# Performance work log

Measured on AMD Instinct MI355X. Metric: run time of the kernel, lower is better.

The kernel has to match this reference:

```python
import jax, jax.numpy as jnp
import numpy as np
import math

N_HEAD = 16

def _rope_tables(seq, dh, dtype):
    inv_freq = 1.0 / (10000.0 ** (jnp.arange(0, dh, 2, dtype=jnp.float32) / dh))
    angle = jnp.arange(seq, dtype=jnp.float32)[:, None] * inv_freq[None, :]  # [S, dh/2]
    sin = jnp.repeat(jnp.sin(angle), 2, axis=-1).astype(dtype)  # [S, dh]
    cos = jnp.repeat(jnp.cos(angle), 2, axis=-1).astype(dtype)
    return sin, cos

def _rotate_half(x):
    x_even = x[..., ::2]
    x_odd = x[..., 1::2]
    return jnp.stack([-x_odd, x_even], axis=-1).reshape(x.shape)

def _apply_rope(x, sin, cos):
    # x: [B, H, S, dh]; sin/cos: [S, dh]
    return x * cos[None, None] + _rotate_half(x) * sin[None, None]

def setup_inputs() -> dict:
    key = jax.random.key(0)
    ks = jax.random.split(key, 9)
    B, S, D = 2, 2048, 2048
    scale = 1.0 / math.sqrt(D)
    x = jax.random.normal(ks[0], (B, S, D), dtype=jnp.float32)
    wq = jax.random.normal(ks[1], (D, D), dtype=jnp.float32) * scale
    wk = jax.random.normal(ks[2], (D, D), dtype=jnp.float32) * scale
    wv = jax.random.normal(ks[3], (D, D), dtype=jnp.float32) * scale
    wo = jax.random.normal(ks[4], (D, D), dtype=jnp.float32) * scale
    bq = jnp.zeros((D,), jnp.float32)
    bk = jnp.zeros((D,), jnp.float32)
    bv = jnp.zeros((D,), jnp.float32)
    bo = jnp.zeros((D,), jnp.float32)
    # causal mask: True = masked (strict upper triangle)
    mask = jnp.triu(jnp.ones((S, S), dtype=bool), k=1)[None, None]  # [1,1,S,S]
    return {"x": x, "wq": wq, "bq": bq, "wk": wk, "bk": bk, "wv": wv, "bv": bv,
            "wo": wo, "bo": bo, "mask": mask}

def reference(x, wq, bq, wk, bk, wv, bv, wo, bo, mask):
    B, S, D = x.shape
    H = N_HEAD
    dh = D // H
    # projections (torch Linear: x @ W.T + b)
    q = (x @ wq.T + bq).reshape(B, S, H, dh).transpose(0, 2, 1, 3)  # [B,H,S,dh]
    k = (x @ wk.T + bk).reshape(B, S, H, dh).transpose(0, 2, 1, 3)
    v = (x @ wv.T + bv).reshape(B, S, H, dh).transpose(0, 2, 1, 3)
    sin, cos = _rope_tables(S, dh, x.dtype)
    q = _apply_rope(q, sin, cos)
    k = _apply_rope(k, sin, cos)
    scores = jnp.einsum('bhqd,bhkd->bhqk', q, k) / math.sqrt(dh)
    scores = jnp.where(mask, -jnp.inf, scores)
    attn = jax.nn.softmax(scores, axis=-1)
    attn = jnp.nan_to_num(attn, nan=0.0)
    out = jnp.einsum('bhqk,bhkd->bhqd', attn, v)  # [B,H,S,dh]
    out = out.transpose(0, 2, 1, 3).reshape(B, S, D)
    return out @ wo.T + bo
```

## Files before the change

kernel.cpp:

```cpp
#include <hip/hip_runtime.h>
#include <math.h>


typedef _Float16 half8 __attribute__((ext_vector_type(8)));
typedef _Float16 half4v __attribute__((ext_vector_type(4)));
typedef float f32x4 __attribute__((ext_vector_type(4)));

__device__ __forceinline__ void gl_lds16(const void* g, void* l) {
  __builtin_amdgcn_global_load_lds(
      (const __attribute__((address_space(1))) unsigned int*)g,
      (__attribute__((address_space(3))) unsigned int*)l, 16, 0, 0);
}

__global__ void cast_f32_f16(const float* __restrict__ src, _Float16* __restrict__ dst, int n4) {
  int i = blockIdx.x * blockDim.x + threadIdx.x;
  if (i >= n4) return;
  float4 v = reinterpret_cast<const float4*>(src)[i];
  half4v o;
  o[0] = (_Float16)v.x; o[1] = (_Float16)v.y; o[2] = (_Float16)v.z; o[3] = (_Float16)v.w;
  reinterpret_cast<half4v*>(dst)[i] = o;
}

__global__ void cast_w(const float* __restrict__ w0, const float* __restrict__ w1,
                       const float* __restrict__ w2, const float* __restrict__ w3,
                       _Float16* __restrict__ wdst) {
  const float* s = blockIdx.y == 0 ? w0 : blockIdx.y == 1 ? w1 : blockIdx.y == 2 ? w2 : w3;
  int i = blockIdx.x * blockDim.x + threadIdx.x;
  float4 v = reinterpret_cast<const float4*>(s)[i];
  half4v o;
  o[0] = (_Float16)v.x; o[1] = (_Float16)v.y; o[2] = (_Float16)v.z; o[3] = (_Float16)v.w;
  reinterpret_cast<half4v*>(wdst)[(size_t)blockIdx.y * 1048576 + i] = o;
}

template <bool OUT_F32>
__global__ __launch_bounds__(256, 2) void gemm_bt_big(
    const _Float16* __restrict__ A,
    const _Float16* __restrict__ B,
    const float* __restrict__ b0, const float* __restrict__ b1,
    const float* __restrict__ b2,
    void* __restrict__ Cout,
    int M, int N, int K) {
  __shared__ _Float16 As[2][4096];
  __shared__ _Float16 Bs[2][8192];
  const int bm = blockIdx.y * 128, bn = blockIdx.x * 256;
  const int tid = threadIdx.x;
  const int wave = tid >> 6, lane = tid & 63;
  const int quad = lane >> 4, l16 = lane & 15;
  const int ih = wave >> 1, jh = wave & 1;

  const _Float16* gsrc[6];
  int lofs[6];
#pragma unroll
  for (int p = 0; p < 6; ++p) {
    if (p < 2) {
      int c = p * 256 + tid;
      int cl16 = c & 15, cqd = (c >> 4) & 3, ci = (c >> 6) & 3, ch = c >> 8;
      gsrc[p] = A + (size_t)(bm + ch * 64 + ci * 16 + cl16) * K + cqd * 8;
      lofs[p] = c * 8;
    } else {
      int c = (p - 2) * 256 + tid;
      int cl16 = c & 15, cqd = (c >> 4) & 3, cn = (c >> 6) & 7, cjh = (c >> 9) & 1;
      gsrc[p] = B + (size_t)(bn + cjh * 128 + cn * 16 + cl16) * K + cqd * 8;
      lofs[p] = c * 8;
    }
  }

  f32x4 acc[4][8];
#pragma unroll
  for (int i = 0; i < 4; ++i)
#pragma unroll
    for (int n = 0; n < 8; ++n) acc[i][n] = f32x4{0.f, 0.f, 0.f, 0.f};

#pragma unroll
  for (int p = 0; p < 6; ++p)
    gl_lds16(gsrc[p], (p < 2 ? &As[0][lofs[p]] : &Bs[0][lofs[p]]));

  const int nit = K >> 5;
  for (int it = 0; it < nit; ++it) {
    __syncthreads();
    const int cur = it & 1;
    if (it + 1 < nit) {
      const int nxt = cur ^ 1, ko = (it + 1) * 32;
#pragma unroll
      for (int p = 0; p < 6; ++p)
        gl_lds16(gsrc[p] + ko, (p < 2 ? &As[nxt][lofs[p]] : &Bs[nxt][lofs[p]]));
    }
    half8 af[4], bf[8];
#pragma unroll
    for (int i = 0; i < 4; ++i)
      af[i] = *reinterpret_cast<const half8*>(&As[cur][((ih * 4 + i) * 4 + quad) * 128 + l16 * 8]);
#pragma unroll
    for (int n = 0; n < 8; ++n)
      bf[n] = *reinterpret_cast<const half8*>(&Bs[cur][((jh * 8 + n) * 4 + quad) * 128 + l16 * 8]);
#pragma unroll
    for (int i = 0; i < 4; ++i)
#pragma unroll
      for (int n = 0; n < 8; ++n)
        acc[i][n] = __builtin_amdgcn_mfma_f32_16x16x32_f16(af[i], bf[n], acc[i][n], 0, 0, 0);
  }

  const int wm = ih * 64, wn = jh * 128;
#pragma unroll
  for (int n = 0; n < 8; ++n) {
    const int gc = bn + wn + n * 16 + l16;
    const float* bp = (gc < 2048) ? b0 : (gc < 4096 ? b1 : b2);
    const float bz = bp[gc & 2047];
#pragma unroll
    for (int i = 0; i < 4; ++i) {
#pragma unroll
      for (int r = 0; r < 4; ++r) {
        const int gr = bm + wm + i * 16 + quad * 4 + r;
        float v = acc[i][n][r] + bz;
        if (OUT_F32)
          reinterpret_cast<float*>(Cout)[(size_t)gr * N + gc] = v;
        else
          reinterpret_cast<_Float16*>(Cout)[(size_t)gr * N + gc] = (_Float16)v;
      }
    }
  }
}

template <bool OUT_F32>
__global__ __launch_bounds__(256, 2) void gemm_bt(
    const _Float16* __restrict__ A, const _Float16* __restrict__ B,
    const float* __restrict__ b0, const float* __restrict__ b1,
    const float* __restrict__ b2, void* __restrict__ Cout, int M, int N, int K) {
  __shared__ _Float16 As[2][4096];
  __shared__ _Float16 Bs[2][4096];
  const int bm = blockIdx.y * 128, bn = blockIdx.x * 128;
  const int tid = threadIdx.x;
  const int wave = tid >> 6, lane = tid & 63;
  const int quad = lane >> 4, l16 = lane & 15;
  const int hh = wave >> 1, gg = wave & 1;

  const _Float16* gsrc[4];
  int lofs[4];
#pragma unroll
  for (int p = 0; p < 4; ++p) {
    int c = ((p & 1) * 256 + tid) & 511;
    int cl16 = c & 15, cqd = (c >> 4) & 3, ci = (c >> 6) & 3, ch = c >> 8;
    int grow = ch * 64 + ci * 16 + cl16;
    gsrc[p] = (p < 2 ? A + (size_t)(bm + grow) * K : B + (size_t)(bn + grow) * K) + cqd * 8;
    lofs[p] = c * 8;
  }

  f32x4 acc[4][4];
#pragma unroll
  for (int i = 0; i < 4; ++i)
#pragma unroll
    for (int n = 0; n < 4; ++n) acc[i][n] = f32x4{0.f, 0.f, 0.f, 0.f};

#pragma unroll
  for (int p = 0; p < 4; ++p)
    gl_lds16(gsrc[p], (p < 2 ? &As[0][lofs[p]] : &Bs[0][lofs[p]]));

  const int nit = K >> 5;
  for (int it = 0; it < nit; ++it) {
    __syncthreads();
    const int cur = it & 1;
    if (it + 1 < nit) {
      const int nxt = cur ^ 1, ko = (it + 1) * 32;
#pragma unroll
      for (int p = 0; p < 4; ++p)
        gl_lds16(gsrc[p] + ko, (p < 2 ? &As[nxt][lofs[p]] : &Bs[nxt][lofs[p]]));
    }
    half8 af[4], bf[4];
#pragma unroll
    for (int i = 0; i < 4; ++i)
      af[i] = *reinterpret_cast<const half8*>(&As[cur][((hh * 4 + i) * 4 + quad) * 128 + l16 * 8]);
#pragma unroll
    for (int n = 0; n < 4; ++n)
      bf[n] = *reinterpret_cast<const half8*>(&Bs[cur][((gg * 4 + n) * 4 + quad) * 128 + l16 * 8]);
#pragma unroll
    for (int i = 0; i < 4; ++i)
#pragma unroll
      for (int n = 0; n < 4; ++n)
        acc[i][n] = __builtin_amdgcn_mfma_f32_16x16x32_f16(af[i], bf[n], acc[i][n], 0, 0, 0);
  }

  const int wm = hh * 64, wn = gg * 64;
#pragma unroll
  for (int n = 0; n < 4; ++n) {
    const int gc = bn + wn + n * 16 + l16;
    const float* bp = (gc < 2048) ? b0 : (gc < 4096 ? b1 : b2);
    const float bz = bp[gc & 2047];
#pragma unroll
    for (int i = 0; i < 4; ++i) {
#pragma unroll
      for (int r = 0; r < 4; ++r) {
        const int gr = bm + wm + i * 16 + quad * 4 + r;
        float v = acc[i][n][r] + bz;
        if (OUT_F32)
          reinterpret_cast<float*>(Cout)[(size_t)gr * N + gc] = v;
        else
          reinterpret_cast<_Float16*>(Cout)[(size_t)gr * N + gc] = (_Float16)v;
      }
    }
  }
}

__global__ void rope_inplace(_Float16* __restrict__ qkv, int ngroups) {
  int idx = blockIdx.x * blockDim.x + threadIdx.x;
  if (idx >= ngroups) return;
  int m = idx >> 8;
  int g = idx & 255;
  int s = m & 2047;
  const float scale = 0.088388347648318447f;
  size_t base = (size_t)m * 6144 + g * 8;
  half8 qv = *reinterpret_cast<const half8*>(qkv + base);
  half8 kv = *reinterpret_cast<const half8*>(qkv + base + 2048);
  half8 qo, ko;
#pragma unroll
  for (int j = 0; j < 4; ++j) {
    int i = (g * 4 + j) & 63;
    float ang = (float)s * exp2f(-0.2076205059304601f * (float)i);
    float sn, cs;
    __sincosf(ang, &sn, &cs);
    float e = (float)qv[j * 2], o = (float)qv[j * 2 + 1];
    qo[j * 2]     = (_Float16)((e * cs - o * sn) * scale);
    qo[j * 2 + 1] = (_Float16)((o * cs + e * sn) * scale);
    e = (float)kv[j * 2]; o = (float)kv[j * 2 + 1];
    ko[j * 2]     = (_Float16)(e * cs - o * sn);
    ko[j * 2 + 1] = (_Float16)(o * cs + e * sn);
  }
  *reinterpret_cast<half8*>(qkv + base) = qo;
  *reinterpret_cast<half8*>(qkv + base + 2048) = ko;
}

__global__ __launch_bounds__(256) void transpose_v(const _Float16* __restrict__ qkv,
                                                   _Float16* __restrict__ vt) {
  __shared__ _Float16 t[64][72];
  const int s0 = blockIdx.x * 64;
  const int d0 = blockIdx.y * 64;
  const int bh = blockIdx.z;
  const int b = bh >> 4, h = bh & 15;
  const int tid = threadIdx.x;
#pragma unroll
  for (int p = 0; p < 2; ++p) {
    int chunk = p * 256 + tid;
    int r = chunk >> 3, c8 = (chunk & 7) * 8;
    *reinterpret_cast<half8*>(&t[r][c8]) = *reinterpret_cast<const half8*>(
        &qkv[(size_t)(b * 2048 + s0 + r) * 6144 + 4096 + h * 128 + d0 + c8]);
  }
  __syncthreads();
#pragma unroll
  for (int p = 0; p < 2; ++p) {
    int chunk = p * 256 + tid;
    int dr = chunk >> 3, c8 = (chunk & 7) * 8;
    half8 o;
#pragma unroll
    for (int j = 0; j < 8; ++j) o[j] = t[c8 + j][dr];
    *reinterpret_cast<half8*>(&vt[(size_t)(bh * 128 + d0 + dr) * 2048 + s0 + c8]) = o;
  }
}

__global__ __launch_bounds__(256, 2) void attn_kernel(
    const _Float16* __restrict__ QKV,
    const _Float16* __restrict__ VT,
    _Float16* __restrict__ ctx) {
  constexpr int LD = 6144, S = 2048;
  __shared__ _Float16 Ks[2][8192];
  __shared__ _Float16 Vs[2][8192];
  __shared__ _Float16 P[4][16][80];
  const int bid = blockIdx.x;
  const int bh = bid & 31;
  const int qt = 15 - (bid >> 5);
  const int b = bh >> 4, h = bh & 15;
  const int tid = threadIdx.x;
  const int wv = tid >> 6, lane = tid & 63;
  const int quad = lane >> 4, l16 = lane & 15;
  const int q0 = qt * 128 + wv * 32;

  half8 aq[2][4];
#pragma unroll
  for (int rt = 0; rt < 2; ++rt)
#pragma unroll
    for (int ks = 0; ks < 4; ++ks)
      aq[rt][ks] = *reinterpret_cast<const half8*>(
          QKV + (size_t)(b * S + q0 + rt * 16 + l16) * LD + h * 128 + ks * 32 + quad * 8);

  const _Float16* gk[4];
  const _Float16* gv[4];
  int lofs[4];
#pragma unroll
  for (int p = 0; p < 4; ++p) {
    int c = p * 256 + tid;
    int cl16 = c & 15, cqd = (c >> 4) & 3;
    int cks = (c >> 6) & 3, cf = c >> 8;
    gk[p] = QKV + (size_t)(b * S + cf * 16 + cl16) * LD + 2048 + h * 128 + cks * 32 + cqd * 8;
    int ckv = (c >> 6) & 1, ct = c >> 7;
    gv[p] = VT + (size_t)(bh * 128 + ct * 16 + cl16) * S + ckv * 32 + cqd * 8;
    lofs[p] = c * 8;
  }

  f32x4 acc[2][8];
#pragma unroll
  for (int rt = 0; rt < 2; ++rt)
#pragma unroll
    for (int t = 0; t < 8; ++t) acc[rt][t] = f32x4{0.f, 0.f, 0.f, 0.f};
  f32x4 lacc[2] = {f32x4{0.f, 0.f, 0.f, 0.f}, f32x4{0.f, 0.f, 0.f, 0.f}};
  float m_i[2][4];
#pragma unroll
  for (int rt = 0; rt < 2; ++rt)
#pragma unroll
    for (int r = 0; r < 4; ++r) m_i[rt][r] = -INFINITY;

  half8 ones;
#pragma unroll
  for (int j = 0; j < 8; ++j) ones[j] = (_Float16)1.0f;

#pragma unroll
  for (int p = 0; p < 4; ++p) gl_lds16(gk[p], &Ks[0][lofs[p]]);
#pragma unroll
  for (int p = 0; p < 4; ++p) gl_lds16(gv[p], &Vs[0][lofs[p]]);

  const int nkt = 2 * (qt + 1);
  for (int j = 0; j < nkt; ++j) {
    __syncthreads();
    const int cur = j & 1;
    if (j + 1 < nkt) {
      const size_t ko = (size_t)(j + 1) * 64 * LD;
      const int vo = (j + 1) * 64;
#pragma unroll
      for (int p = 0; p < 4; ++p) gl_lds16(gk[p] + ko, &Ks[cur ^ 1][lofs[p]]);
#pragma unroll
      for (int p = 0; p < 4; ++p) gl_lds16(gv[p] + vo, &Vs[cur ^ 1][lofs[p]]);
    }
    const int key0 = j * 64;
    if (key0 > q0 + 31) continue;

    f32x4 sf[2][4];
#pragma unroll
    for (int rt = 0; rt < 2; ++rt)
#pragma unroll
      for (int f = 0; f < 4; ++f) sf[rt][f] = f32x4{0.f, 0.f, 0.f, 0.f};
#pragma unroll
    for (int f = 0; f < 4; ++f)
#pragma unroll
      for (int ks = 0; ks < 4; ++ks) {
        half8 bk = *reinterpret_cast<const half8*>(&Ks[cur][((f * 4 + ks) * 4 + quad) * 128 + l16 * 8]);
        sf[0][f] = __builtin_amdgcn_mfma_f32_16x16x32_f16(aq[0][ks], bk, sf[0][f], 0, 0, 0);
        sf[1][f] = __builtin_amdgcn_mfma_f32_16x16x32_f16(aq[1][ks], bk, sf[1][f], 0, 0, 0);
      }
    if (key0 + 63 > q0) {
#pragma unroll
      for (int rt = 0; rt < 2; ++rt)
#pragma unroll
        for (int f = 0; f < 4; ++f) {
          const int key = key0 + f * 16 + l16;
#pragma unroll
          for (int r = 0; r < 4; ++r) {
            const int row = q0 + rt * 16 + quad * 4 + r;
            sf[rt][f][r] = (key <= row) ? sf[rt][f][r] : -1e30f;
          }
        }
    }
    float alpha[2][4];
    half8 pa[2][2];
#pragma unroll
    for (int rt = 0; rt < 2; ++rt) {
#pragma unroll
      for (int r = 0; r < 4; ++r) {
        float tm = fmaxf(fmaxf(sf[rt][0][r], sf[rt][1][r]), fmaxf(sf[rt][2][r], sf[rt][3][r]));
        tm = fmaxf(tm, __shfl_xor(tm, 1));
        tm = fmaxf(tm, __shfl_xor(tm, 2));
        tm = fmaxf(tm, __shfl_xor(tm, 4));
        tm = fmaxf(tm, __shfl_xor(tm, 8));
        const float mn = fmaxf(m_i[rt][r], tm);
        alpha[rt][r] = __expf(m_i[rt][r] - mn);
        m_i[rt][r] = mn;
      }
#pragma unroll
      for (int f = 0; f < 4; ++f)
#pragma unroll
        for (int r = 0; r < 4; ++r)
          P[wv][quad * 4 + r][f * 16 + l16] = (_Float16)__expf(sf[rt][f][r] - m_i[rt][r]);
      pa[rt][0] = *reinterpret_cast<const half8*>(&P[wv][l16][quad * 8]);
      pa[rt][1] = *reinterpret_cast<const half8*>(&P[wv][l16][32 + quad * 8]);
    }
#pragma unroll
    for (int rt = 0; rt < 2; ++rt) {
#pragma unroll
      for (int t = 0; t < 8; ++t)
#pragma unroll
        for (int r = 0; r < 4; ++r) acc[rt][t][r] *= alpha[rt][r];
#pragma unroll
      for (int r = 0; r < 4; ++r) lacc[rt][r] *= alpha[rt][r];
    }
#pragma unroll
    for (int t = 0; t < 8; ++t) {
      half8 bv0 = *reinterpret_cast<const half8*>(&Vs[cur][((t * 2 + 0) * 4 + quad) * 128 + l16 * 8]);
      half8 bv1 = *reinterpret_cast<const half8*>(&Vs[cur][((t * 2 + 1) * 4 + quad) * 128 + l16 * 8]);
#pragma unroll
      for (int rt = 0; rt < 2; ++rt) {
        acc[rt][t] = __builtin_amdgcn_mfma_f32_16x16x32_f16(pa[rt][0], bv0, acc[rt][t], 0, 0, 0);
        acc[rt][t] = __builtin_amdgcn_mfma_f32_16x16x32_f16(pa[rt][1], bv1, acc[rt][t], 0, 0, 0);
      }
    }
#pragma unroll
    for (int rt = 0; rt < 2; ++rt) {
      lacc[rt] = __builtin_amdgcn_mfma_f32_16x16x32_f16(pa[rt][0], ones, lacc[rt], 0, 0, 0);
      lacc[rt] = __builtin_amdgcn_mfma_f32_16x16x32_f16(pa[rt][1], ones, lacc[rt], 0, 0, 0);
    }
  }

#pragma unroll
  for (int rt = 0; rt < 2; ++rt) {
    float inv[4];
#pragma unroll
    for (int r = 0; r < 4; ++r) inv[r] = 1.0f / lacc[rt][r];
#pragma unroll
    for (int t = 0; t < 8; ++t)
#pragma unroll
      for (int r = 0; r < 4; ++r)
        ctx[(size_t)(b * S + q0 + rt * 16 + quad * 4 + r) * 2048 + h * 128 + t * 16 + l16] =
            (_Float16)(acc[rt][t][r] * inv[r]);
  }
}

extern "C" void kernel_launch(void* const* d_in, const int* in_sizes, int n_in,
                              void* d_out, int out_size, void* d_ws, size_t ws_size,
                              hipStream_t stream) {
  const float* x  = (const float*)d_in[0];
  const float* wq = (const float*)d_in[1];
  const float* bq = (const float*)d_in[2];
  const float* wk = (const float*)d_in[3];
  const float* bk = (const float*)d_in[4];
  const float* wv = (const float*)d_in[5];
  const float* bv = (const float*)d_in[6];
  const float* wo = (const float*)d_in[7];
  const float* bo = (const float*)d_in[8];

  _Float16* W      = (_Float16*)d_ws;
  _Float16* xh     = W;
  _Float16* wqkvh  = xh + 8388608;
  _Float16* woh    = wqkvh + 12582912;
  _Float16* qkvlin = woh + 4194304;
  _Float16* vT     = xh;
  _Float16* ctx    = wqkvh;

  cast_f32_f16<<<8192, 256, 0, stream>>>(x, xh, 2097152);
  cast_w<<<dim3(4096, 4), 256, 0, stream>>>(wq, wk, wv, wo, wqkvh);

  gemm_bt_big<false><<<dim3(24, 32), 256, 0, stream>>>(xh, wqkvh, bq, bk, bv, qkvlin,
                                                       4096, 6144, 2048);

  rope_inplace<<<4096, 256, 0, stream>>>(qkvlin, 1048576);
  transpose_v<<<dim3(32, 2, 32), 256, 0, stream>>>(qkvlin, vT);
  attn_kernel<<<512, 256, 0, stream>>>(qkvlin, vT, ctx);

  gemm_bt<true><<<dim3(16, 32), 256, 0, stream>>>(ctx, woh, bo, bo, bo, (float*)d_out,
                                                  4096, 2048, 2048);
}
```

Measured before the change: 526.1 us.

## Replace LDS-staged GEMMs with direct global-to-register loads and register double buffering

Both projection GEMMs now use one 128x128 kernel that reads MFMA fragments straight from global memory into registers, with two register sets as a software pipeline. This drops the LDS staging, the per-iteration barriers and the separate 128x256 variant. The launch grid becomes 1D with M-fastest block ordering, so consecutive blocks share B tiles in cache, and occupancy is raised to 3 blocks per CU. The cost is that each wave issues many small strided 16-byte global loads and operand data is no longer shared between waves, so more traffic goes through L1/L2.

```diff
diff --git a/kernel.cpp b/kernel.cpp
--- a/kernel.cpp
+++ b/kernel.cpp
@@ -33,116 +33,22 @@
 }
 
 template <bool OUT_F32>
-__global__ __launch_bounds__(256, 2) void gemm_bt_big(
+__global__ __launch_bounds__(256, 3) void gemm_bt(
     const _Float16* __restrict__ A,
     const _Float16* __restrict__ B,
     const float* __restrict__ b0, const float* __restrict__ b1,
     const float* __restrict__ b2,
     void* __restrict__ Cout,
-    int M, int N, int K) {
-  __shared__ _Float16 As[2][4096];
-  __shared__ _Float16 Bs[2][8192];
-  const int bm = blockIdx.y * 128, bn = blockIdx.x * 256;
-  const int tid = threadIdx.x;
-  const int wave = tid >> 6, lane = tid & 63;
-  const int quad = lane >> 4, l16 = lane & 15;
-  const int ih = wave >> 1, jh = wave & 1;
-
-  const _Float16* gsrc[6];
-  int lofs[6];
-#pragma unroll
-  for (int p = 0; p < 6; ++p) {
-    if (p < 2) {
-      int c = p * 256 + tid;
-      int cl16 = c & 15, cqd = (c >> 4) & 3, ci = (c >> 6) & 3, ch = c >> 8;
-      gsrc[p] = A + (size_t)(bm + ch * 64 + ci * 16 + cl16) * K + cqd * 8;
-      lofs[p] = c * 8;
-    } else {
-      int c = (p - 2) * 256 + tid;
-      int cl16 = c & 15, cqd = (c >> 4) & 3, cn = (c >> 6) & 7, cjh = (c >> 9) & 1;
-      gsrc[p] = B + (size_t)(bn + cjh * 128 + cn * 16 + cl16) * K + cqd * 8;
-      lofs[p] = c * 8;
-    }
-  }
-
-  f32x4 acc[4][8];
-#pragma unroll
-  for (int i = 0; i < 4; ++i)
-#pragma unroll
-    for (int n = 0; n < 8; ++n) acc[i][n] = f32x4{0.f, 0.f, 0.f, 0.f};
-
-#pragma unroll
-  for (int p = 0; p < 6; ++p)
-    gl_lds16(gsrc[p], (p < 2 ? &As[0][lofs[p]] : &Bs[0][lofs[p]]));
-
-  const int nit = K >> 5;
-  for (int it = 0; it < nit; ++it) {
-    __syncthreads();
-    const int cur = it & 1;
-    if (it + 1 < nit) {
-      const int nxt = cur ^ 1, ko = (it + 1) * 32;
-#pragma unroll
-      for (int p = 0; p < 6; ++p)
-        gl_lds16(gsrc[p] + ko, (p < 2 ? &As[nxt][lofs[p]] : &Bs[nxt][lofs[p]]));
-    }
-    half8 af[4], bf[8];
-#pragma unroll
-    for (int i = 0; i < 4; ++i)
-      af[i] = *reinterpret_cast<const half8*>(&As[cur][((ih * 4 + i) * 4 + quad) * 128 + l16 * 8]);
-#pragma unroll
-    for (int n = 0; n < 8; ++n)
-      bf[n] = *reinterpret_cast<const half8*>(&Bs[cur][((jh * 8 + n) * 4 + quad) * 128 + l16 * 8]);
-#pragma unroll
-    for (int i = 0; i < 4; ++i)
-#pragma unroll
-      for (int n = 0; n < 8; ++n)
-        acc[i][n] = __builtin_amdgcn_mfma_f32_16x16x32_f16(af[i], bf[n], acc[i][n], 0, 0, 0);
-  }
-
-  const int wm = ih * 64, wn = jh * 128;
-#pragma unroll
-  for (int n = 0; n < 8; ++n) {
-    const int gc = bn + wn + n * 16 + l16;
-    const float* bp = (gc < 2048) ? b0 : (gc < 4096 ? b1 : b2);
-    const float bz = bp[gc & 2047];
-#pragma unroll
-    for (int i = 0; i < 4; ++i) {
-#pragma unroll
-      for (int r = 0; r < 4; ++r) {
-        const int gr = bm + wm + i * 16 + quad * 4 + r;
-        float v = acc[i][n][r] + bz;
-        if (OUT_F32)
-          reinterpret_cast<float*>(Cout)[(size_t)gr * N + gc] = v;
-        else
-          reinterpret_cast<_Float16*>(Cout)[(size_t)gr * N + gc] = (_Float16)v;
-      }
-    }
-  }
-}
-
-template <bool OUT_F32>
-__global__ __launch_bounds__(256, 2) void gemm_bt(
-    const _Float16* __restrict__ A, const _Float16* __restrict__ B,
-    const float* __restrict__ b0, const float* __restrict__ b1,
-    const float* __restrict__ b2, void* __restrict__ Cout, int M, int N, int K) {
-  __shared__ _Float16 As[2][4096];
-  __shared__ _Float16 Bs[2][4096];
-  const int bm = blockIdx.y * 128, bn = blockIdx.x * 128;
-  const int tid = threadIdx.x;
-  const int wave = tid >> 6, lane = tid & 63;
+    int N) {
+  constexpr int K = 2048;
+  const int bid = blockIdx.x;
+  const int bm = (bid & 31) * 128, bn = (bid >> 5) * 128;
+  const int wave = threadIdx.x >> 6, lane = threadIdx.x & 63;
   const int quad = lane >> 4, l16 = lane & 15;
   const int hh = wave >> 1, gg = wave & 1;
 
-  const _Float16* gsrc[4];
-  int lofs[4];
-#pragma unroll
-  for (int p = 0; p < 4; ++p) {
-    int c = ((p & 1) * 256 + tid) & 511;
-    int cl16 = c & 15, cqd = (c >> 4) & 3, ci = (c >> 6) & 3, ch = c >> 8;
-    int grow = ch * 64 + ci * 16 + cl16;
-    gsrc[p] = (p < 2 ? A + (size_t)(bm + grow) * K : B + (size_t)(bn + grow) * K) + cqd * 8;
-    lofs[p] = c * 8;
-  }
+  const _Float16* pA = A + (size_t)(bm + hh * 64 + l16) * K + quad * 8;
+  const _Float16* pB = B + (size_t)(bn + gg * 64 + l16) * K + quad * 8;
 
   f32x4 acc[4][4];
 #pragma unroll
@@ -150,33 +56,33 @@
 #pragma unroll
     for (int n = 0; n < 4; ++n) acc[i][n] = f32x4{0.f, 0.f, 0.f, 0.f};
 
-#pragma unroll
-  for (int p = 0; p < 4; ++p)
-    gl_lds16(gsrc[p], (p < 2 ? &As[0][lofs[p]] : &Bs[0][lofs[p]]));
-
-  const int nit = K >> 5;
-  for (int it = 0; it < nit; ++it) {
-    __syncthreads();
-    const int cur = it & 1;
-    if (it + 1 < nit) {
-      const int nxt = cur ^ 1, ko = (it + 1) * 32;
-#pragma unroll
-      for (int p = 0; p < 4; ++p)
-        gl_lds16(gsrc[p] + ko, (p < 2 ? &As[nxt][lofs[p]] : &Bs[nxt][lofs[p]]));
-    }
-    half8 af[4], bf[4];
+  auto ld = [&](half8* fa, half8* fb, int ko) {
 #pragma unroll
     for (int i = 0; i < 4; ++i)
-      af[i] = *reinterpret_cast<const half8*>(&As[cur][((hh * 4 + i) * 4 + quad) * 128 + l16 * 8]);
+      fa[i] = *reinterpret_cast<const half8*>(pA + (size_t)i * 16 * K + ko);
 #pragma unroll
     for (int n = 0; n < 4; ++n)
-      bf[n] = *reinterpret_cast<const half8*>(&Bs[cur][((gg * 4 + n) * 4 + quad) * 128 + l16 * 8]);
+      fb[n] = *reinterpret_cast<const half8*>(pB + (size_t)n * 16 * K + ko);
+  };
+  auto mm = [&](const half8* fa, const half8* fb) {
 #pragma unroll
     for (int i = 0; i < 4; ++i)
 #pragma unroll
       for (int n = 0; n < 4; ++n)
-        acc[i][n] = __builtin_amdgcn_mfma_f32_16x16x32_f16(af[i], bf[n], acc[i][n], 0, 0, 0);
-  }
+        acc[i][n] = __builtin_amdgcn_mfma_f32_16x16x32_f16(fa[i], fb[n], acc[i][n], 0, 0, 0);
+  };
+
+  half8 fa0[4], fb0[4], fa1[4], fb1[4];
+  ld(fa0, fb0, 0);
+  for (int it = 0; it < (K / 32) - 2; it += 2) {
+    ld(fa1, fb1, (it + 1) * 32);
+    mm(fa0, fb0);
+    ld(fa0, fb0, (it + 2) * 32);
+    mm(fa1, fb1);
+  }
+  ld(fa1, fb1, (K / 32 - 1) * 32);
+  mm(fa0, fb0);
+  mm(fa1, fb1);
 
   const int wm = hh * 64, wn = gg * 64;
 #pragma unroll
@@ -442,13 +348,11 @@
   cast_f32_f16<<<8192, 256, 0, stream>>>(x, xh, 2097152);
   cast_w<<<dim3(4096, 4), 256, 0, stream>>>(wq, wk, wv, wo, wqkvh);
 
-  gemm_bt_big<false><<<dim3(24, 32), 256, 0, stream>>>(xh, wqkvh, bq, bk, bv, qkvlin,
-                                                       4096, 6144, 2048);
+  gemm_bt<false><<<1536, 256, 0, stream>>>(xh, wqkvh, bq, bk, bv, qkvlin, 6144);
 
   rope_inplace<<<4096, 256, 0, stream>>>(qkvlin, 1048576);
   transpose_v<<<dim3(32, 2, 32), 256, 0, stream>>>(qkvlin, vT);
   attn_kernel<<<512, 256, 0, stream>>>(qkvlin, vT, ctx);
 
-  gemm_bt<true><<<dim3(16, 32), 256, 0, stream>>>(ctx, woh, bo, bo, bo, (float*)d_out,
-                                                  4096, 2048, 2048);
-}
+  gemm_bt<true><<<512, 256, 0, stream>>>(ctx, woh, bo, bo, bo, (float*)d_out, 2048);
+}
```

Result: slower. 747.9 us (+42.2%).
